# Optimization experiments

Hardware: AMD Instinct MI355X
Metric: run time of the kernel (lower is better)

The kernel has to match this reference:

```python
import jax, jax.numpy as jnp
import numpy as np

B, S, D_IN, D_H = 8, 2048, 512, 512

def setup_inputs() -> dict:
    key = jax.random.key(0)
    ks = jax.random.split(key, 7)
    scale = 1.0 / np.sqrt(D_IN)
    return {
        "x": jax.random.normal(ks[0], (B, S, D_IN), dtype=jnp.float32),
        "Wq": jax.random.uniform(ks[1], (D_IN, D_H), jnp.float32, -scale, scale),
        "bq": jax.random.uniform(ks[2], (D_H,), jnp.float32, -scale, scale),
        "Wk": jax.random.uniform(ks[3], (D_IN, D_H), jnp.float32, -scale, scale),
        "bk": jax.random.uniform(ks[4], (D_H,), jnp.float32, -scale, scale),
        "Wv": jax.random.uniform(ks[5], (D_IN, D_H), jnp.float32, -scale, scale),
        "bv": jax.random.uniform(ks[6], (D_H,), jnp.float32, -scale, scale),
    }

def reference(x, Wq, bq, Wk, bk, Wv, bv):
    q = jnp.einsum("bsd,dh->bsh", x, Wq) + bq  # [B,S,H]
    k = jnp.einsum("bsd,dh->bsh", x, Wk) + bk
    v = jnp.einsum("bsd,dh->bsh", x, Wv) + bv
    # NOTE: original has NO 1/sqrt(d) scaling — faithful reproduction
    scores = jnp.einsum("bqh,bkh->bqk", q, k)  # [B,S,S]
    probs = jax.nn.softmax(scores, axis=-1)
    return jnp.einsum("bqk,bkh->bqh", probs, v)
```

## Files before the change

### kernel.cpp

```cpp
#include <hip/hip_runtime.h>


typedef __attribute__((ext_vector_type(8))) _Float16 f16x8;
typedef __attribute__((ext_vector_type(8))) short bf16x8;
typedef __attribute__((ext_vector_type(4))) float f32x4;

__device__ __forceinline__ unsigned short f2h(float f) {
  _Float16 h = (_Float16)f;
  return *(unsigned short*)&h;
}
__device__ __forceinline__ unsigned short f2bf(float f) {
  unsigned int u = __float_as_uint(f);
  unsigned int r = (u + 0x7fffu + ((u >> 16) & 1u)) >> 16;
  return (unsigned short)r;
}
__device__ __forceinline__ float bf2f(unsigned short h) {
  return __uint_as_float(((unsigned int)h) << 16);
}

__device__ __forceinline__ void load_lds16(const void* g, void* l) {
  __builtin_amdgcn_global_load_lds(
      (const __attribute__((address_space(1))) unsigned int*)g,
      (__attribute__((address_space(3))) unsigned int*)l, 16, 0, 0);
}

__global__ __launch_bounds__(256) void convx_kernel(const float* __restrict__ x,
                                                    unsigned short* __restrict__ xh) {
  int i = blockIdx.x * 256 + threadIdx.x;
  float4 v = ((const float4*)x)[i];
  union { unsigned short h[4]; short4 s4; } u;
  u.h[0] = f2h(v.x); u.h[1] = f2h(v.y); u.h[2] = f2h(v.z); u.h[3] = f2h(v.w);
  ((short4*)xh)[i] = u.s4;
}

__global__ __launch_bounds__(256) void convw_kernel(
    const float* __restrict__ W0, const float* __restrict__ W1,
    const float* __restrict__ W2, unsigned short* __restrict__ Wt) {
  const float* W = (blockIdx.z == 0) ? W0 : (blockIdx.z == 1) ? W1 : W2;
  unsigned short* t = Wt + (size_t)blockIdx.z * 512 * 512;
  __shared__ float tile[32][33];
  int tx = threadIdx.x, ty = threadIdx.y;
  int h0 = blockIdx.x * 32, d0 = blockIdx.y * 32;
  for (int i = ty; i < 32; i += 8) tile[i][tx] = W[(long)(d0 + i) * 512 + h0 + tx];
  __syncthreads();
  for (int i = ty; i < 32; i += 8)
    t[(long)(h0 + i) * 512 + d0 + tx] = f2h(tile[tx][i]);
}

__global__ __launch_bounds__(256) void gemm_qkv_kernel(
    const unsigned short* __restrict__ A,
    const unsigned short* __restrict__ Bt,
    unsigned short* __restrict__ Qo, unsigned short* __restrict__ Ko,
    unsigned short* __restrict__ VTo,
    const float* __restrict__ bq, const float* __restrict__ bk,
    const float* __restrict__ bv) {
  __shared__ alignas(16) unsigned short As[128 * 32];
  __shared__ alignas(16) unsigned short Bs[128 * 32];
  const int t = threadIdx.x;
  const long long bm = (long long)blockIdx.x * 128;
  const long long bn = (long long)blockIdx.y * 128;

  const int ar = t >> 2;
  const int ac = (t & 3) * 8;

  f32x4 acc[4][4];
#pragma unroll
  for (int i = 0; i < 4; i++)
#pragma unroll
    for (int j = 0; j < 4; j++) acc[i][j] = {0.f, 0.f, 0.f, 0.f};

  const int lane = t & 63;
  const int wave = t >> 6;
  const int wm = (wave & 1) * 64;
  const int wn = (wave >> 1) * 64;
  const int fm = lane & 15;
  const int k8 = (lane >> 4) * 8;

  for (int kt = 0; kt < 512; kt += 32) {
#pragma unroll
    for (int r = 0; r < 2; r++)
      load_lds16(A + (bm + r * 64 + ar) * 512 + kt + ac, &As[r * 2048 + t * 8]);
#pragma unroll
    for (int r = 0; r < 2; r++)
      load_lds16(Bt + (bn + r * 64 + ar) * 512 + kt + ac, &Bs[r * 2048 + t * 8]);
    __syncthreads();

    f16x8 af[4], bfr[4];
#pragma unroll
    for (int i = 0; i < 4; i++)
      af[i] = *(const f16x8*)&As[(wm + i * 16 + fm) * 32 + k8];
#pragma unroll
    for (int j = 0; j < 4; j++)
      bfr[j] = *(const f16x8*)&Bs[(wn + j * 16 + fm) * 32 + k8];
#pragma unroll
    for (int i = 0; i < 4; i++)
#pragma unroll
      for (int j = 0; j < 4; j++)
        acc[i][j] = __builtin_amdgcn_mfma_f32_16x16x32_f16(af[i], bfr[j], acc[i][j], 0, 0, 0);
    __syncthreads();
  }

  const int crow = (lane >> 4) * 4;
  const int ccol = lane & 15;
#pragma unroll
  for (int j = 0; j < 4; j++) {
    const long long col = bn + wn + j * 16 + ccol;
    float bias = (col < 512) ? bq[col] : (col < 1024) ? bk[col - 512] : bv[col - 1024];
#pragma unroll
    for (int i = 0; i < 4; i++) {
      const long long row0 = bm + wm + i * 16 + crow;
      if (col >= 1024) {
        const long long b = row0 >> 11;
        const long long s = row0 & 2047;
        union { unsigned short h[4]; short4 s4; } u;
#pragma unroll
        for (int r = 0; r < 4; r++) u.h[r] = f2bf(acc[i][j][r] + bias);
        *(short4*)(VTo + (b * 512 + (col - 1024)) * 2048 + s) = u.s4;
      } else {
        unsigned short* dst = (col < 512) ? (Qo + row0 * 512 + col)
                                          : (Ko + row0 * 512 + (col - 512));
#pragma unroll
        for (int r = 0; r < 4; r++) dst[(size_t)r * 512] = f2h(acc[i][j][r] + bias);
      }
    }
  }
}

__global__ __launch_bounds__(256) void gemm_pexp_kernel(
    const unsigned short* __restrict__ Qg,
    const unsigned short* __restrict__ Kg,
    unsigned short* __restrict__ P,
    float* __restrict__ rowsum) {
  __shared__ alignas(16) unsigned short As[128 * 32];
  __shared__ alignas(16) unsigned short Bs[128 * 32];
  const int t = threadIdx.x;
  const long long bm = (long long)blockIdx.x * 128;
  const long long bn = (long long)blockIdx.y * 128;
  const int z = blockIdx.z;
  const unsigned short* Ab = Qg + (size_t)z * 2048 * 512;
  const unsigned short* Bb = Kg + (size_t)z * 2048 * 512;

  const int ar = t >> 2;
  const int ac = (t & 3) * 8;

  f32x4 acc[4][4];
#pragma unroll
  for (int i = 0; i < 4; i++)
#pragma unroll
    for (int j = 0; j < 4; j++) acc[i][j] = {0.f, 0.f, 0.f, 0.f};

  const int lane = t & 63;
  const int wave = t >> 6;
  const int wm = (wave & 1) * 64;
  const int wn = (wave >> 1) * 64;
  const int fm = lane & 15;
  const int k8 = (lane >> 4) * 8;

  for (int kt = 0; kt < 512; kt += 32) {
#pragma unroll
    for (int r = 0; r < 2; r++)
      load_lds16(Ab + (bm + r * 64 + ar) * 512 + kt + ac, &As[r * 2048 + t * 8]);
#pragma unroll
    for (int r = 0; r < 2; r++)
      load_lds16(Bb + (bn + r * 64 + ar) * 512 + kt + ac, &Bs[r * 2048 + t * 8]);
    __syncthreads();

    f16x8 af[4], bfr[4];
#pragma unroll
    for (int i = 0; i < 4; i++)
      af[i] = *(const f16x8*)&As[(wm + i * 16 + fm) * 32 + k8];
#pragma unroll
    for (int j = 0; j < 4; j++)
      bfr[j] = *(const f16x8*)&Bs[(wn + j * 16 + fm) * 32 + k8];
#pragma unroll
    for (int i = 0; i < 4; i++)
#pragma unroll
      for (int j = 0; j < 4; j++)
        acc[i][j] = __builtin_amdgcn_mfma_f32_16x16x32_f16(af[i], bfr[j], acc[i][j], 0, 0, 0);
    __syncthreads();
  }

  unsigned short* Pb = P + (size_t)z * 2048 * 2048;
  const int quad = lane >> 4;
  const int crow = quad * 4;
  const int ccol = lane & 15;
  float psum[4][4];
#pragma unroll
  for (int i = 0; i < 4; i++)
#pragma unroll
    for (int r = 0; r < 4; r++) psum[i][r] = 0.f;
#pragma unroll
  for (int j = 0; j < 4; j++) {
    const long long col = bn + wn + j * 16 + ccol;
#pragma unroll
    for (int i = 0; i < 4; i++) {
      const long long row0 = bm + wm + i * 16 + crow;
#pragma unroll
      for (int r = 0; r < 4; r++) {
        unsigned short pb = f2bf(__expf(acc[i][j][r]));
        Pb[(row0 + r) * 2048 + col] = pb;
        psum[i][r] += bf2f(pb);
      }
    }
  }
#pragma unroll
  for (int off = 1; off < 16; off <<= 1)
#pragma unroll
    for (int i = 0; i < 4; i++)
#pragma unroll
      for (int r = 0; r < 4; r++) psum[i][r] += __shfl_xor(psum[i][r], off);
  if ((lane & 15) == 0) {
    float* rs = rowsum + (size_t)z * 2048;
#pragma unroll
    for (int i = 0; i < 4; i++) {
      const long long row0 = bm + wm + i * 16 + crow;
#pragma unroll
      for (int r = 0; r < 4; r++) atomicAdd(&rs[row0 + r], psum[i][r]);
    }
  }
}

__global__ __launch_bounds__(256) void gemm_pv_kernel(
    const unsigned short* __restrict__ P,
    const unsigned short* __restrict__ Vt,
    const float* __restrict__ rowsum,
    float* __restrict__ out) {
  __shared__ alignas(16) unsigned short As[128 * 32];
  __shared__ alignas(16) unsigned short Bs[128 * 32];
  const int t = threadIdx.x;
  const long long bm = (long long)blockIdx.x * 128;
  const long long bn = (long long)blockIdx.y * 128;
  const int z = blockIdx.z;
  const unsigned short* Ab = P + (size_t)z * 2048 * 2048;
  const unsigned short* Bb = Vt + (size_t)z * 512 * 2048;

  const int ar = t >> 2;
  const int ac = (t & 3) * 8;

  f32x4 acc[4][4];
#pragma unroll
  for (int i = 0; i < 4; i++)
#pragma unroll
    for (int j = 0; j < 4; j++) acc[i][j] = {0.f, 0.f, 0.f, 0.f};

  const int lane = t & 63;
  const int wave = t >> 6;
  const int wm = (wave & 1) * 64;
  const int wn = (wave >> 1) * 64;
  const int fm = lane & 15;
  const int k8 = (lane >> 4) * 8;

  for (int kt = 0; kt < 2048; kt += 32) {
#pragma unroll
    for (int r = 0; r < 2; r++)
      load_lds16(Ab + (bm + r * 64 + ar) * 2048 + kt + ac, &As[r * 2048 + t * 8]);
#pragma unroll
    for (int r = 0; r < 2; r++)
      load_lds16(Bb + (bn + r * 64 + ar) * 2048 + kt + ac, &Bs[r * 2048 + t * 8]);
    __syncthreads();

    bf16x8 af[4], bfr[4];
#pragma unroll
    for (int i = 0; i < 4; i++)
      af[i] = *(const bf16x8*)&As[(wm + i * 16 + fm) * 32 + k8];
#pragma unroll
    for (int j = 0; j < 4; j++)
      bfr[j] = *(const bf16x8*)&Bs[(wn + j * 16 + fm) * 32 + k8];
#pragma unroll
    for (int i = 0; i < 4; i++)
#pragma unroll
      for (int j = 0; j < 4; j++)
        acc[i][j] = __builtin_amdgcn_mfma_f32_16x16x32_bf16(af[i], bfr[j], acc[i][j], 0, 0, 0);
    __syncthreads();
  }

  float* ob = out + (size_t)z * 2048 * 512;
  const float* rs = rowsum + (size_t)z * 2048;
  const int crow = (lane >> 4) * 4;
  const int ccol = lane & 15;
  float inv[4][4];
#pragma unroll
  for (int i = 0; i < 4; i++) {
    const long long row0 = bm + wm + i * 16 + crow;
#pragma unroll
    for (int r = 0; r < 4; r++) inv[i][r] = 1.0f / rs[row0 + r];
  }
#pragma unroll
  for (int j = 0; j < 4; j++) {
    const long long col = bn + wn + j * 16 + ccol;
#pragma unroll
    for (int i = 0; i < 4; i++) {
      const long long row0 = bm + wm + i * 16 + crow;
#pragma unroll
      for (int r = 0; r < 4; r++)
        ob[(row0 + r) * 512 + col] = acc[i][j][r] * inv[i][r];
    }
  }
}

extern "C" void kernel_launch(void* const* d_in, const int* in_sizes, int n_in,
                              void* d_out, int out_size, void* d_ws, size_t ws_size,
                              hipStream_t stream) {
  const float* x  = (const float*)d_in[0];
  const float* Wq = (const float*)d_in[1];
  const float* bq = (const float*)d_in[2];
  const float* Wk = (const float*)d_in[3];
  const float* bk = (const float*)d_in[4];
  const float* Wv = (const float*)d_in[5];
  const float* bv = (const float*)d_in[6];
  float* out = (float*)d_out;

  const size_t SZ = (size_t)16384 * 512 * 2;
  char* p = (char*)d_ws;
  unsigned short* xh = (unsigned short*)p; p += SZ;
  unsigned short* Wt = (unsigned short*)p; p += (size_t)3 * 512 * 512 * 2;
  unsigned short* Qb = (unsigned short*)p; p += SZ;
  unsigned short* Kb = (unsigned short*)p; p += SZ;
  unsigned short* VT = (unsigned short*)p; p += SZ;
  float* rowsum = (float*)p; p += (size_t)16384 * 4;
  unsigned short* P = (unsigned short*)p; p += (size_t)8 * 2048 * 2048 * 2;

  hipMemsetAsync(rowsum, 0, 16384 * sizeof(float), stream);
  convx_kernel<<<8192, 256, 0, stream>>>(x, xh);
  convw_kernel<<<dim3(16, 16, 3), dim3(32, 8), 0, stream>>>(Wq, Wk, Wv, Wt);
  gemm_qkv_kernel<<<dim3(128, 12), 256, 0, stream>>>(xh, Wt, Qb, Kb, VT, bq, bk, bv);
  gemm_pexp_kernel<<<dim3(16, 16, 8), 256, 0, stream>>>(Qb, Kb, P, rowsum);
  gemm_pv_kernel<<<dim3(16, 4, 8), 256, 0, stream>>>(P, VT, rowsum, out);
}
```

Baseline: 261.2 us.

## Fuse QK^T exp and PV into a single flash-style attention kernel

Replaces the separate QK-exp kernel, which wrote an 8x2048x2048 bf16 P matrix plus atomic row sums, and the PV kernel with one fused kernel. Each block keeps 32 query rows in LDS and streams K and V straight from global memory into registers. It computes exp scores into a swizzled LDS tile and accumulates P·V in registers, normalising at the end. This removes the large P round-trip through HBM, the memset and the atomics. In exchange the grid shrinks to 512 blocks of 4 waves and K/V are re-read from global or L2 by every query block without LDS staging. Like the earlier code, it applies exp without subtracting a row max.

Result: slower. 373.2 us (+42.9%).

```diff
diff --git a/kernel.cpp b/kernel.cpp
--- a/kernel.cpp
+++ b/kernel.cpp
@@ -126,174 +126,149 @@
   }
 }
 
-__global__ __launch_bounds__(256) void gemm_pexp_kernel(
+__global__ __launch_bounds__(256) void attn_fused_kernel(
     const unsigned short* __restrict__ Qg,
     const unsigned short* __restrict__ Kg,
-    unsigned short* __restrict__ P,
-    float* __restrict__ rowsum) {
-  __shared__ alignas(16) unsigned short As[128 * 32];
-  __shared__ alignas(16) unsigned short Bs[128 * 32];
+    const unsigned short* __restrict__ Vg,
+    float* __restrict__ out) {
+  __shared__ alignas(16) unsigned short Qs[32 * 512];
+  __shared__ alignas(16) unsigned short Ps[32 * 128];
+  __shared__ float rsw[4][32];
+
   const int t = threadIdx.x;
-  const long long bm = (long long)blockIdx.x * 128;
-  const long long bn = (long long)blockIdx.y * 128;
-  const int z = blockIdx.z;
-  const unsigned short* Ab = Qg + (size_t)z * 2048 * 512;
-  const unsigned short* Bb = Kg + (size_t)z * 2048 * 512;
-
-  const int ar = t >> 2;
-  const int ac = (t & 3) * 8;
-
-  f32x4 acc[4][4];
-#pragma unroll
-  for (int i = 0; i < 4; i++)
-#pragma unroll
-    for (int j = 0; j < 4; j++) acc[i][j] = {0.f, 0.f, 0.f, 0.f};
-
   const int lane = t & 63;
-  const int wave = t >> 6;
-  const int wm = (wave & 1) * 64;
-  const int wn = (wave >> 1) * 64;
+  const int w = t >> 6;
   const int fm = lane & 15;
-  const int k8 = (lane >> 4) * 8;
-
-  for (int kt = 0; kt < 512; kt += 32) {
-#pragma unroll
-    for (int r = 0; r < 2; r++)
-      load_lds16(Ab + (bm + r * 64 + ar) * 512 + kt + ac, &As[r * 2048 + t * 8]);
-#pragma unroll
-    for (int r = 0; r < 2; r++)
-      load_lds16(Bb + (bn + r * 64 + ar) * 512 + kt + ac, &Bs[r * 2048 + t * 8]);
+  const int g = lane >> 4;
+  const int b = blockIdx.x & 7;
+  const int q0 = (blockIdx.x >> 3) << 5;
+
+  const unsigned short* Qb = Qg + ((size_t)b * 2048 + q0) * 512;
+  const unsigned short* Kb = Kg + (size_t)b * 2048 * 512;
+  const unsigned short* Vb = Vg + (size_t)b * 512 * 2048;
+
+#pragma unroll
+  for (int c = 0; c < 8; ++c) {
+    const int L = c * 4096 + t * 16;
+    const int q = L >> 10;
+    const int o = (L & 1023) ^ ((q & 7) << 4);
+    load_lds16(Qb + (size_t)q * 512 + (o >> 1), &Qs[L >> 1]);
+  }
+
+  f32x4 oacc[2][8];
+#pragma unroll
+  for (int i = 0; i < 2; ++i)
+#pragma unroll
+    for (int j = 0; j < 8; ++j) oacc[i][j] = {0.f, 0.f, 0.f, 0.f};
+  float rsv0 = 0.f, rsv1 = 0.f;
+
+  const int sx = (fm >> 2) & 1;
+  const int s45 = (fm & 3) << 4;
+  const int gx = (g * 16) ^ s45;
+  const int qA = (0 * 16 + fm) * 1024 + gx;
+  const int qB = (1 * 16 + fm) * 1024 + gx;
+  const int pA = (0 * 16 + fm) * 256 + gx;
+  const int pB = (1 * 16 + fm) * 256 + gx;
+
+  __syncthreads();
+
+  for (int kt = 0; kt < 2048; kt += 128) {
+    const unsigned short* Kw = Kb + (size_t)(kt + w * 32) * 512 + g * 8;
+    const unsigned short* Kr0 = Kw + (size_t)fm * 512;
+    const unsigned short* Kr1 = Kw + (size_t)(16 + fm) * 512;
+
+    f32x4 sacc[2][2];
+#pragma unroll
+    for (int i = 0; i < 2; ++i)
+#pragma unroll
+      for (int j = 0; j < 2; ++j) sacc[i][j] = {0.f, 0.f, 0.f, 0.f};
+
+    f16x8 ka0 = *(const f16x8*)Kr0;
+    f16x8 ka1 = *(const f16x8*)Kr1;
+#pragma unroll
+    for (int ds = 0; ds < 16; ++ds) {
+      const f16x8 a0 = ka0, a1 = ka1;
+      if (ds < 15) {
+        ka0 = *(const f16x8*)(Kr0 + (ds + 1) * 32);
+        ka1 = *(const f16x8*)(Kr1 + (ds + 1) * 32);
+      }
+      const int dz = (ds ^ sx) << 6;
+      const f16x8 qf0 = *(const f16x8*)((const char*)Qs + qA + dz);
+      const f16x8 qf1 = *(const f16x8*)((const char*)Qs + qB + dz);
+      sacc[0][0] = __builtin_amdgcn_mfma_f32_16x16x32_f16(a0, qf0, sacc[0][0], 0, 0, 0);
+      sacc[0][1] = __builtin_amdgcn_mfma_f32_16x16x32_f16(a0, qf1, sacc[0][1], 0, 0, 0);
+      sacc[1][0] = __builtin_amdgcn_mfma_f32_16x16x32_f16(a1, qf0, sacc[1][0], 0, 0, 0);
+      sacc[1][1] = __builtin_amdgcn_mfma_f32_16x16x32_f16(a1, qf1, sacc[1][1], 0, 0, 0);
+    }
+
+#pragma unroll
+    for (int i = 0; i < 2; ++i) {
+      const int kb2 = w * 64 + i * 32 + g * 8;
+#pragma unroll
+      for (int j = 0; j < 2; ++j) {
+        const int q = j * 16 + fm;
+        union { unsigned short h[4]; short4 s4; } u;
+        float s0 = 0.f;
+#pragma unroll
+        for (int r = 0; r < 4; ++r) {
+          const unsigned short pb = f2bf(__expf(sacc[i][j][r]));
+          u.h[r] = pb;
+          s0 += bf2f(pb);
+        }
+        if (j == 0) rsv0 += s0; else rsv1 += s0;
+        *(short4*)((char*)Ps + q * 256 + (kb2 ^ ((q & 7) << 4))) = u.s4;
+      }
+    }
+
+    const unsigned short* Vw = Vb + (size_t)(w * 128 + fm) * 2048 + kt + g * 8;
+    bf16x8 vfn[8];
+#pragma unroll
+    for (int j = 0; j < 8; ++j)
+      vfn[j] = *(const bf16x8*)(Vw + (size_t)(j * 16) * 2048);
     __syncthreads();
 
-    f16x8 af[4], bfr[4];
-#pragma unroll
-    for (int i = 0; i < 4; i++)
-      af[i] = *(const f16x8*)&As[(wm + i * 16 + fm) * 32 + k8];
-#pragma unroll
-    for (int j = 0; j < 4; j++)
-      bfr[j] = *(const f16x8*)&Bs[(wn + j * 16 + fm) * 32 + k8];
-#pragma unroll
-    for (int i = 0; i < 4; i++)
-#pragma unroll
-      for (int j = 0; j < 4; j++)
-        acc[i][j] = __builtin_amdgcn_mfma_f32_16x16x32_f16(af[i], bfr[j], acc[i][j], 0, 0, 0);
+#pragma unroll
+    for (int ks = 0; ks < 4; ++ks) {
+      bf16x8 vf[8];
+#pragma unroll
+      for (int j = 0; j < 8; ++j) vf[j] = vfn[j];
+      if (ks < 3) {
+#pragma unroll
+        for (int j = 0; j < 8; ++j)
+          vfn[j] = *(const bf16x8*)(Vw + (size_t)(j * 16) * 2048 + (ks + 1) * 32);
+      }
+      const int kz = (ks ^ sx) << 6;
+      const bf16x8 pf0 = *(const bf16x8*)((const char*)Ps + pA + kz);
+      const bf16x8 pf1 = *(const bf16x8*)((const char*)Ps + pB + kz);
+#pragma unroll
+      for (int j = 0; j < 8; ++j) {
+        oacc[0][j] = __builtin_amdgcn_mfma_f32_16x16x32_bf16(pf0, vf[j], oacc[0][j], 0, 0, 0);
+        oacc[1][j] = __builtin_amdgcn_mfma_f32_16x16x32_bf16(pf1, vf[j], oacc[1][j], 0, 0, 0);
+      }
+    }
     __syncthreads();
   }
 
-  unsigned short* Pb = P + (size_t)z * 2048 * 2048;
-  const int quad = lane >> 4;
-  const int crow = quad * 4;
-  const int ccol = lane & 15;
-  float psum[4][4];
-#pragma unroll
-  for (int i = 0; i < 4; i++)
-#pragma unroll
-    for (int r = 0; r < 4; r++) psum[i][r] = 0.f;
-#pragma unroll
-  for (int j = 0; j < 4; j++) {
-    const long long col = bn + wn + j * 16 + ccol;
-#pragma unroll
-    for (int i = 0; i < 4; i++) {
-      const long long row0 = bm + wm + i * 16 + crow;
-#pragma unroll
-      for (int r = 0; r < 4; r++) {
-        unsigned short pb = f2bf(__expf(acc[i][j][r]));
-        Pb[(row0 + r) * 2048 + col] = pb;
-        psum[i][r] += bf2f(pb);
-      }
-    }
-  }
-#pragma unroll
-  for (int off = 1; off < 16; off <<= 1)
-#pragma unroll
-    for (int i = 0; i < 4; i++)
-#pragma unroll
-      for (int r = 0; r < 4; r++) psum[i][r] += __shfl_xor(psum[i][r], off);
-  if ((lane & 15) == 0) {
-    float* rs = rowsum + (size_t)z * 2048;
-#pragma unroll
-    for (int i = 0; i < 4; i++) {
-      const long long row0 = bm + wm + i * 16 + crow;
-#pragma unroll
-      for (int r = 0; r < 4; r++) atomicAdd(&rs[row0 + r], psum[i][r]);
-    }
-  }
-}
-
-__global__ __launch_bounds__(256) void gemm_pv_kernel(
-    const unsigned short* __restrict__ P,
-    const unsigned short* __restrict__ Vt,
-    const float* __restrict__ rowsum,
-    float* __restrict__ out) {
-  __shared__ alignas(16) unsigned short As[128 * 32];
-  __shared__ alignas(16) unsigned short Bs[128 * 32];
-  const int t = threadIdx.x;
-  const long long bm = (long long)blockIdx.x * 128;
-  const long long bn = (long long)blockIdx.y * 128;
-  const int z = blockIdx.z;
-  const unsigned short* Ab = P + (size_t)z * 2048 * 2048;
-  const unsigned short* Bb = Vt + (size_t)z * 512 * 2048;
-
-  const int ar = t >> 2;
-  const int ac = (t & 3) * 8;
-
-  f32x4 acc[4][4];
-#pragma unroll
-  for (int i = 0; i < 4; i++)
-#pragma unroll
-    for (int j = 0; j < 4; j++) acc[i][j] = {0.f, 0.f, 0.f, 0.f};
-
-  const int lane = t & 63;
-  const int wave = t >> 6;
-  const int wm = (wave & 1) * 64;
-  const int wn = (wave >> 1) * 64;
-  const int fm = lane & 15;
-  const int k8 = (lane >> 4) * 8;
-
-  for (int kt = 0; kt < 2048; kt += 32) {
-#pragma unroll
-    for (int r = 0; r < 2; r++)
-      load_lds16(Ab + (bm + r * 64 + ar) * 2048 + kt + ac, &As[r * 2048 + t * 8]);
-#pragma unroll
-    for (int r = 0; r < 2; r++)
-      load_lds16(Bb + (bn + r * 64 + ar) * 2048 + kt + ac, &Bs[r * 2048 + t * 8]);
-    __syncthreads();
-
-    bf16x8 af[4], bfr[4];
-#pragma unroll
-    for (int i = 0; i < 4; i++)
-      af[i] = *(const bf16x8*)&As[(wm + i * 16 + fm) * 32 + k8];
-#pragma unroll
-    for (int j = 0; j < 4; j++)
-      bfr[j] = *(const bf16x8*)&Bs[(wn + j * 16 + fm) * 32 + k8];
-#pragma unroll
-    for (int i = 0; i < 4; i++)
-#pragma unroll
-      for (int j = 0; j < 4; j++)
-        acc[i][j] = __builtin_amdgcn_mfma_f32_16x16x32_bf16(af[i], bfr[j], acc[i][j], 0, 0, 0);
-    __syncthreads();
-  }
-
-  float* ob = out + (size_t)z * 2048 * 512;
-  const float* rs = rowsum + (size_t)z * 2048;
-  const int crow = (lane >> 4) * 4;
-  const int ccol = lane & 15;
-  float inv[4][4];
-#pragma unroll
-  for (int i = 0; i < 4; i++) {
-    const long long row0 = bm + wm + i * 16 + crow;
-#pragma unroll
-    for (int r = 0; r < 4; r++) inv[i][r] = 1.0f / rs[row0 + r];
-  }
-#pragma unroll
-  for (int j = 0; j < 4; j++) {
-    const long long col = bn + wn + j * 16 + ccol;
-#pragma unroll
-    for (int i = 0; i < 4; i++) {
-      const long long row0 = bm + wm + i * 16 + crow;
-#pragma unroll
-      for (int r = 0; r < 4; r++)
-        ob[(row0 + r) * 512 + col] = acc[i][j][r] * inv[i][r];
+  rsv0 += __shfl_xor(rsv0, 16); rsv0 += __shfl_xor(rsv0, 32);
+  rsv1 += __shfl_xor(rsv1, 16); rsv1 += __shfl_xor(rsv1, 32);
+  if (g == 0) { rsw[w][fm] = rsv0; rsw[w][16 + fm] = rsv1; }
+  __syncthreads();
+
+  float* ob = out + ((size_t)b * 2048 + q0) * 512;
+#pragma unroll
+  for (int i = 0; i < 2; ++i) {
+    float inv[4];
+#pragma unroll
+    for (int r = 0; r < 4; ++r) {
+      const int q = i * 16 + g * 4 + r;
+      inv[r] = 1.0f / (rsw[0][q] + rsw[1][q] + rsw[2][q] + rsw[3][q]);
+    }
+#pragma unroll
+    for (int j = 0; j < 8; ++j) {
+      const int d = w * 128 + j * 16 + fm;
+#pragma unroll
+      for (int r = 0; r < 4; ++r)
+        ob[(size_t)(i * 16 + g * 4 + r) * 512 + d] = oacc[i][j][r] * inv[r];
     }
   }
 }
@@ -317,13 +292,9 @@
   unsigned short* Qb = (unsigned short*)p; p += SZ;
   unsigned short* Kb = (unsigned short*)p; p += SZ;
   unsigned short* VT = (unsigned short*)p; p += SZ;
-  float* rowsum = (float*)p; p += (size_t)16384 * 4;
-  unsigned short* P = (unsigned short*)p; p += (size_t)8 * 2048 * 2048 * 2;
-
-  hipMemsetAsync(rowsum, 0, 16384 * sizeof(float), stream);
+
   convx_kernel<<<8192, 256, 0, stream>>>(x, xh);
   convw_kernel<<<dim3(16, 16, 3), dim3(32, 8), 0, stream>>>(Wq, Wk, Wv, Wt);
   gemm_qkv_kernel<<<dim3(128, 12), 256, 0, stream>>>(xh, Wt, Qb, Kb, VT, bq, bk, bv);
-  gemm_pexp_kernel<<<dim3(16, 16, 8), 256, 0, stream>>>(Qb, Kb, P, rowsum);
-  gemm_pv_kernel<<<dim3(16, 4, 8), 256, 0, stream>>>(P, VT, rowsum, out);
-}
+  attn_fused_kernel<<<512, 256, 0, stream>>>(Qb, Kb, VT, out);
+}
```
